# Kernel tuning notes

Hardware: AMD Instinct MI355X
Metric: run time of the kernel (lower is better)

The kernel has to match this reference:

```python
import jax, jax.numpy as jnp
import numpy as np

N, K, DIM, A, M = 20000, 16, 256, 128, 2500
EPS = 1e-5
SCALE = float(np.sqrt(A))


def _ln(x, g, b):
    mu = x.mean(-1, keepdims=True)
    var = x.var(-1, keepdims=True)
    return (x - mu) / jnp.sqrt(var + EPS) * g + b


def _pe(x, w1, b1, w2, b2):
    # PositionEncoder: Linear -> ReLU -> Linear
    return jax.nn.relu(x @ w1 + b1) @ w2 + b2


def setup_inputs() -> dict:
    key = jax.random.key(0)
    ks = jax.random.split(key, 24)
    w = lambda k, s, fan: jax.random.normal(k, s, jnp.float32) / np.sqrt(fan)
    inp = {
        'events': jax.random.normal(ks[0], (N, 4), jnp.float32),
        'features': jax.random.normal(ks[1], (N, DIM), jnp.float32),
        'local_idx': jax.random.randint(ks[2], (N, K), 0, N, jnp.int32),
        'down_idx': jax.random.randint(ks[3], (M,), 0, N, jnp.int32),
        'pair_idx': jax.random.randint(ks[4], (M, K), 0, N, jnp.int32),
        'inv_pair_idx': jax.random.randint(ks[5], (N, K), 0, M, jnp.int32),
        'local_qkv_w': w(ks[6], (DIM, 3 * A), DIM), 'local_qkv_b': jnp.zeros((3 * A,), jnp.float32),
        'local_pe_w1': w(ks[7], (4, A), 4), 'local_pe_b1': jnp.zeros((A,), jnp.float32),
        'local_pe_w2': w(ks[8], (A, A), A), 'local_pe_b2': jnp.zeros((A,), jnp.float32),
        'local_fc_g': jnp.ones((A,), jnp.float32), 'local_fc_b': jnp.zeros((A,), jnp.float32),
        'global_qkv_w': w(ks[9], (DIM, 3 * A), DIM), 'global_qkv_b': jnp.zeros((3 * A,), jnp.float32),
        'global_pe_w1': w(ks[10], (4, A), 4), 'global_pe_b1': jnp.zeros((A,), jnp.float32),
        'global_pe_w2': w(ks[11], (A, A), A), 'global_pe_b2': jnp.zeros((A,), jnp.float32),
        'global_fc_g': jnp.ones((A,), jnp.float32), 'global_fc_b': jnp.zeros((A,), jnp.float32),
        'proj_w1': w(ks[12], (2 * A, DIM), 2 * A), 'proj_b1': jnp.zeros((DIM,), jnp.float32),
        'proj_w2': w(ks[13], (DIM, DIM), DIM), 'proj_b2': jnp.zeros((DIM,), jnp.float32),
    }
    return inp


def _local_attn(events, features, local_idx, qkv_w, qkv_b,
                pe_w1, pe_b1, pe_w2, pe_b2, fc_g, fc_b):
    # pos enc on event-coordinate differences to the 16 knn neighbors
    pe = _pe(events[:, None, :] - events[local_idx], pe_w1, pe_b1, pe_w2, pe_b2)  # [N,K,A]
    qkv = features @ qkv_w + qkv_b
    q, k, v = jnp.split(qkv, 3, axis=-1)               # [N,A] each
    kg, vg = k[local_idx], v[local_idx]                # [N,K,A]
    attn = _ln(q[:, None, :] - kg + pe, fc_g, fc_b) / SCALE
    attn = jax.nn.softmax(attn, axis=1)                # softmax over neighbors
    return jnp.sum(attn * (vg + pe), axis=1)           # [N,A]


def _global_attn(events, features, down_idx, pair_idx, inv_pair_idx,
                 qkv_w, qkv_b, pe_w1, pe_b1, pe_w2, pe_b2, fc_g, fc_b):
    down_events = events[down_idx]                     # [M,4]
    pe = _pe(events[:, None, :] - down_events[inv_pair_idx], pe_w1, pe_b1, pe_w2, pe_b2)  # [N,K,A]
    qkv = features @ qkv_w + qkv_b
    q, k, v = jnp.split(qkv, 3, axis=-1)
    kmax = jnp.max(k[pair_idx], axis=1)                # [M,A] pooled over k support pts
    vmax = jnp.max(v[pair_idx], axis=1)
    kg, vg = kmax[inv_pair_idx], vmax[inv_pair_idx]    # [N,K,A]
    attn = _ln(q[:, None, :] - kg + pe, fc_g, fc_b) / SCALE
    attn = jax.nn.softmax(attn, axis=1)
    return jnp.sum(attn * (vg + pe), axis=1)


def reference(events, features, local_idx, down_idx, pair_idx, inv_pair_idx,
              local_qkv_w, local_qkv_b, local_pe_w1, local_pe_b1, local_pe_w2, local_pe_b2,
              local_fc_g, local_fc_b,
              global_qkv_w, global_qkv_b, global_pe_w1, global_pe_b1, global_pe_w2, global_pe_b2,
              global_fc_g, global_fc_b,
              proj_w1, proj_b1, proj_w2, proj_b2):
    la = _local_attn(events, features, local_idx, local_qkv_w, local_qkv_b,
                     local_pe_w1, local_pe_b1, local_pe_w2, local_pe_b2,
                     local_fc_g, local_fc_b)
    ga = _global_attn(events, features, down_idx, pair_idx, inv_pair_idx,
                      global_qkv_w, global_qkv_b, global_pe_w1, global_pe_b1,
                      global_pe_w2, global_pe_b2, global_fc_g, global_fc_b)
    attn = jnp.concatenate([la, ga], axis=-1)          # [N,2A]
    # proj MLP: Linear -> ReLU -> Linear
    return jax.nn.relu(attn @ proj_w1 + proj_b1) @ proj_w2 + proj_b2
```

## Files before the change

### kernel.cpp

```cpp
#include <hip/hip_runtime.h>

#define N_PTS 20000
#define KNN   16
#define DIMF  256
#define AD    128
#define MD    2500
#define EPSV  1e-5f
#define INV_SCALE 0.08838834764831845f
#define NEG_BIG -3.402823466e38f

typedef __attribute__((ext_vector_type(8))) short short8v;
typedef __attribute__((ext_vector_type(4))) float f32x4;

__device__ __forceinline__ float b2f(unsigned short u) {
  union { unsigned int i; float f; } v; v.i = ((unsigned int)u) << 16; return v.f;
}
__device__ __forceinline__ unsigned short f2b(float f) {
  union { float f; unsigned int i; } v; v.f = f;
  unsigned int x = v.i;
  return (unsigned short)((x + 0x7fffu + ((x >> 16) & 1u)) >> 16);
}

__global__ void EventAttention_54382875902362_kernel(float* out) {
  if (threadIdx.x == 0 && blockIdx.x == 0) out[0] = 8192.0f;
}

__global__ void prep_w2(const float* __restrict__ w2l, const float* __restrict__ w2g,
                        unsigned short* __restrict__ w2B)
{
  int id  = blockIdx.x * 256 + threadIdx.x;
  int br  = id >> 14;
  int rem = id & 16383;
  int e  = rem & 7;
  int l  = (rem >> 3) & 63;
  int ks = (rem >> 9) & 3;
  int tt = rem >> 11;
  int n = tt * 16 + (l & 15);
  int i = ks * 32 + (l >> 4) * 8 + e;
  const float* src = br ? w2g : w2l;
  w2B[id] = f2b(src[i * AD + n]);
}

__global__ void prep_frag(const float* __restrict__ src, unsigned short* __restrict__ dst,
                          int ncols, int frag_elems)
{
  int id = blockIdx.x * 256 + threadIdx.x;
  if (id >= frag_elems) return;
  int e  = id & 7;
  int l  = (id >> 3) & 63;
  int ks = (id >> 9) & 7;
  int tt = id >> 12;
  int n = tt * 16 + (l & 15);
  int k = ks * 32 + (l >> 4) * 8 + e;
  float v = src[k * ncols + n];
  unsigned short hi = f2b(v);
  unsigned short lo = f2b(v - b2f(hi));
  dst[id] = hi;
  dst[frag_elems + id] = lo;
}

__global__ void qkv_mfma(const float* __restrict__ feat,
                         const unsigned short* __restrict__ wfl, const float* __restrict__ bl,
                         const unsigned short* __restrict__ wfg, const float* __restrict__ bg,
                         float* __restrict__ qkv_l, float* __restrict__ qkv_g)
{
  __shared__ __align__(16) unsigned short aHi[16 * 256];
  __shared__ __align__(16) unsigned short aLo[16 * 256];
  const int tid  = threadIdx.x;
  const int lane = tid & 63;
  const int wv   = tid >> 6;
  const int br   = blockIdx.x & 1;
  const int row0 = (blockIdx.x >> 1) * 16;

  {
    int r = tid >> 4, seg = tid & 15;
    const float4* src = (const float4*)(feat + (size_t)(row0 + r) * 256 + seg * 16);
    #pragma unroll
    for (int q4 = 0; q4 < 4; ++q4) {
      float4 f = src[q4];
      int byte = (r * 512 + (seg * 16 + q4 * 4) * 2) ^ ((r & 7) << 4);
      ushort4 h, l2;
      h.x = f2b(f.x); l2.x = f2b(f.x - b2f(h.x));
      h.y = f2b(f.y); l2.y = f2b(f.y - b2f(h.y));
      h.z = f2b(f.z); l2.z = f2b(f.z - b2f(h.z));
      h.w = f2b(f.w); l2.w = f2b(f.w - b2f(h.w));
      *(ushort4*)((char*)aHi + byte) = h;
      *(ushort4*)((char*)aLo + byte) = l2;
    }
  }
  __syncthreads();

  short8v ah[8], al[8];
  #pragma unroll
  for (int ks = 0; ks < 8; ++ks) {
    int base = ((lane & 15) * 512 + ks * 64 + (lane >> 4) * 16) ^ ((lane & 7) << 4);
    ah[ks] = *(const short8v*)((const char*)aHi + base);
    al[ks] = *(const short8v*)((const char*)aLo + base);
  }
  const unsigned short* wf = br ? wfg : wfl;
  const float* bias        = br ? bg : bl;
  float* outp              = br ? qkv_g : qkv_l;
  const short8v* wH = (const short8v*)wf;
  const short8v* wL = wH + 12288;
  f32x4 acc[6];
  #pragma unroll
  for (int t = 0; t < 6; ++t) acc[t] = (f32x4){0.f, 0.f, 0.f, 0.f};
  #pragma unroll
  for (int t = 0; t < 6; ++t) {
    int tt = wv * 6 + t;
    #pragma unroll
    for (int ks = 0; ks < 8; ++ks) {
      short8v bh = wH[(tt * 8 + ks) * 64 + lane];
      short8v bo = wL[(tt * 8 + ks) * 64 + lane];
      acc[t] = __builtin_amdgcn_mfma_f32_16x16x32_bf16(ah[ks], bh, acc[t], 0, 0, 0);
      acc[t] = __builtin_amdgcn_mfma_f32_16x16x32_bf16(al[ks], bh, acc[t], 0, 0, 0);
      acc[t] = __builtin_amdgcn_mfma_f32_16x16x32_bf16(ah[ks], bo, acc[t], 0, 0, 0);
    }
  }
  #pragma unroll
  for (int t = 0; t < 6; ++t) {
    int colb = (wv * 6 + t) * 16 + (lane & 15);
    float bv = bias[colb];
    #pragma unroll
    for (int r = 0; r < 4; ++r) {
      int row = (lane >> 4) * 4 + r;
      outp[(size_t)(row0 + row) * 384 + colb] = acc[t][r] + bv;
    }
  }
}

__global__ void kvmax_kernel(const float* __restrict__ qkv_g,
                             const int* __restrict__ pair_idx,
                             float* __restrict__ kmax, float* __restrict__ vmax)
{
  const int m = blockIdx.x, a = threadIdx.x;
  float km = NEG_BIG, vm = NEG_BIG;
  for (int j = 0; j < KNN; ++j) {
    int p = pair_idx[m * KNN + j];
    km = fmaxf(km, qkv_g[(size_t)p * 384 + 128 + a]);
    vm = fmaxf(vm, qkv_g[(size_t)p * 384 + 256 + a]);
  }
  kmax[m * AD + a] = km;
  vmax[m * AD + a] = vm;
}

__global__ void attn_kernel(const float* __restrict__ events,
                            const int* __restrict__ idx,
                            const int* __restrict__ remap, int use_remap,
                            const float* __restrict__ q_tab, int qstride,
                            const float* __restrict__ k_tab, int kstride,
                            const float* __restrict__ v_tab, int vstride,
                            const float* __restrict__ w1, const float* __restrict__ b1,
                            const unsigned short* __restrict__ w2B, const float* __restrict__ b2,
                            const float* __restrict__ g,  const float* __restrict__ bb,
                            float* __restrict__ out, int out_off)
{
  __shared__ __align__(16) unsigned short hB[KNN * AD];
  __shared__ float scratch[KNN * 132];
  __shared__ float dS[KNN][4];
  __shared__ int   idxS[KNN];
  __shared__ float red[2][KNN][2];

  const int n    = blockIdx.x;
  const int a    = threadIdx.x;
  const int lane = a & 63;
  const int wv   = a >> 6;

  if (a < KNN * 4) {
    int j = a >> 2, c = a & 3;
    int id = idx[n * KNN + j];
    if (c == 0) idxS[j] = id;
    int erow = use_remap ? remap[id] : id;
    dS[j][c] = events[(size_t)n * 4 + c] - events[(size_t)erow * 4 + c];
  }
  const float w1r0 = w1[0 * AD + a];
  const float w1r1 = w1[1 * AD + a];
  const float w1r2 = w1[2 * AD + a];
  const float w1r3 = w1[3 * AD + a];
  const float b1r = b1[a];
  const float b2r = b2[a];
  __syncthreads();

  #pragma unroll
  for (int j = 0; j < KNN; ++j) {
    float h = b1r;
    h = fmaf(dS[j][0], w1r0, h);
    h = fmaf(dS[j][1], w1r1, h);
    h = fmaf(dS[j][2], w1r2, h);
    h = fmaf(dS[j][3], w1r3, h);
    h = fmaxf(h, 0.f);
    int byte = (j * 256 + a * 2) ^ ((j & 7) << 4);
    *(unsigned short*)((char*)hB + byte) = f2b(h);
  }
  __syncthreads();

  short8v af[4];
  #pragma unroll
  for (int ks = 0; ks < 4; ++ks) {
    int base = ((lane & 15) * 256 + ks * 64 + (lane >> 4) * 16) ^ ((lane & 7) << 4);
    af[ks] = *(const short8v*)((const char*)hB + base);
  }
  f32x4 acc[4];
  #pragma unroll
  for (int t = 0; t < 4; ++t) acc[t] = (f32x4){0.f, 0.f, 0.f, 0.f};
  const short8v* wf = (const short8v*)w2B;
  #pragma unroll
  for (int t = 0; t < 4; ++t) {
    #pragma unroll
    for (int ks = 0; ks < 4; ++ks) {
      short8v bf = wf[(((wv * 4 + t) * 4 + ks) * 64) + lane];
      acc[t] = __builtin_amdgcn_mfma_f32_16x16x32_bf16(af[ks], bf, acc[t], 0, 0, 0);
    }
  }
  #pragma unroll
  for (int t = 0; t < 4; ++t) {
    #pragma unroll
    for (int r = 0; r < 4; ++r) {
      int row = (lane >> 4) * 4 + r;
      int col = wv * 64 + t * 16 + (lane & 15);
      scratch[row * 132 + col] = acc[t][r];
    }
  }
  __syncthreads();

  float pe[KNN];
  #pragma unroll
  for (int j = 0; j < KNN; ++j) pe[j] = scratch[j * 132 + a] + b2r;

  const float qv = q_tab[(size_t)n * qstride + a];
  float x[KNN];
  #pragma unroll
  for (int j = 0; j < KNN; ++j) {
    float kg = k_tab[(size_t)idxS[j] * kstride + a];
    x[j] = qv - kg + pe[j];
  }
  __syncthreads();

  #pragma unroll
  for (int j = 0; j < KNN; ++j) scratch[j * 129 + a] = x[j];
  __syncthreads();

  {
    int jj = a & 15, pp = a >> 4;
    float s1 = 0.f, s2 = 0.f;
    #pragma unroll
    for (int c = 0; c < 16; ++c) {
      float v = scratch[jj * 129 + pp * 16 + c];
      s1 += v;
      s2 += v * v;
    }
    s1 += __shfl_xor(s1, 16, 64); s2 += __shfl_xor(s2, 16, 64);
    s1 += __shfl_xor(s1, 32, 64); s2 += __shfl_xor(s2, 32, 64);
    if (lane < 16) { red[wv][jj][0] = s1; red[wv][jj][1] = s2; }
  }
  __syncthreads();

  const float gr = g[a], br = bb[a];
  float mx = NEG_BIG;
  #pragma unroll
  for (int j = 0; j < KNN; ++j) {
    float S1 = red[0][j][0] + red[1][j][0];
    float S2 = red[0][j][1] + red[1][j][1];
    float mu  = S1 * (1.f / AD);
    float var = S2 * (1.f / AD) - mu * mu;
    float rs  = rsqrtf(var + EPSV);
    float s = ((x[j] - mu) * rs * gr + br) * INV_SCALE;
    x[j] = s;
    mx = fmaxf(mx, s);
  }
  float sum = 0.f;
  #pragma unroll
  for (int j = 0; j < KNN; ++j) {
    float p = __expf(x[j] - mx);
    x[j] = p;
    sum += p;
  }
  const float inv = 1.f / sum;
  float o = 0.f;
  #pragma unroll
  for (int j = 0; j < KNN; ++j) {
    float vg = v_tab[(size_t)idxS[j] * vstride + a];
    o += x[j] * (vg + pe[j]);
  }
  out[(size_t)n * 256 + out_off + a] = o * inv;
}

__global__ void proj_mfma(const float* __restrict__ attn_cat,
                          const unsigned short* __restrict__ w1f, const float* __restrict__ b1,
                          const unsigned short* __restrict__ w2f, const float* __restrict__ b2,
                          float* __restrict__ outp)
{
  __shared__ __align__(16) unsigned short aHi[16 * 256];
  __shared__ __align__(16) unsigned short aLo[16 * 256];
  const int tid  = threadIdx.x;
  const int lane = tid & 63;
  const int wv   = tid >> 6;
  const int row0 = blockIdx.x * 16;

  {
    int r = tid >> 4, seg = tid & 15;
    const float4* src = (const float4*)(attn_cat + (size_t)(row0 + r) * 256 + seg * 16);
    #pragma unroll
    for (int q4 = 0; q4 < 4; ++q4) {
      float4 f = src[q4];
      int byte = (r * 512 + (seg * 16 + q4 * 4) * 2) ^ ((r & 7) << 4);
      ushort4 h, l2;
      h.x = f2b(f.x); l2.x = f2b(f.x - b2f(h.x));
      h.y = f2b(f.y); l2.y = f2b(f.y - b2f(h.y));
      h.z = f2b(f.z); l2.z = f2b(f.z - b2f(h.z));
      h.w = f2b(f.w); l2.w = f2b(f.w - b2f(h.w));
      *(ushort4*)((char*)aHi + byte) = h;
      *(ushort4*)((char*)aLo + byte) = l2;
    }
  }
  __syncthreads();

  short8v ah[8], al[8];
  #pragma unroll
  for (int ks = 0; ks < 8; ++ks) {
    int base = ((lane & 15) * 512 + ks * 64 + (lane >> 4) * 16) ^ ((lane & 7) << 4);
    ah[ks] = *(const short8v*)((const char*)aHi + base);
    al[ks] = *(const short8v*)((const char*)aLo + base);
  }
  __syncthreads();

  const short8v* w1H = (const short8v*)w1f;
  const short8v* w1L = w1H + 8192;
  f32x4 acc[4];
  #pragma unroll
  for (int t = 0; t < 4; ++t) acc[t] = (f32x4){0.f, 0.f, 0.f, 0.f};
  #pragma unroll
  for (int t = 0; t < 4; ++t) {
    int tt = wv * 4 + t;
    #pragma unroll
    for (int ks = 0; ks < 8; ++ks) {
      short8v bh = w1H[(tt * 8 + ks) * 64 + lane];
      short8v bo = w1L[(tt * 8 + ks) * 64 + lane];
      acc[t] = __builtin_amdgcn_mfma_f32_16x16x32_bf16(ah[ks], bh, acc[t], 0, 0, 0);
      acc[t] = __builtin_amdgcn_mfma_f32_16x16x32_bf16(al[ks], bh, acc[t], 0, 0, 0);
      acc[t] = __builtin_amdgcn_mfma_f32_16x16x32_bf16(ah[ks], bo, acc[t], 0, 0, 0);
    }
  }
  #pragma unroll
  for (int t = 0; t < 4; ++t) {
    int col = (wv * 4 + t) * 16 + (lane & 15);
    float bv = b1[col];
    #pragma unroll
    for (int r = 0; r < 4; ++r) {
      int row = (lane >> 4) * 4 + r;
      float h = fmaxf(acc[t][r] + bv, 0.f);
      unsigned short hi = f2b(h);
      unsigned short lo = f2b(h - b2f(hi));
      int byte = (row * 512 + col * 2) ^ ((row & 7) << 4);
      *(unsigned short*)((char*)aHi + byte) = hi;
      *(unsigned short*)((char*)aLo + byte) = lo;
    }
  }
  __syncthreads();

  #pragma unroll
  for (int ks = 0; ks < 8; ++ks) {
    int base = ((lane & 15) * 512 + ks * 64 + (lane >> 4) * 16) ^ ((lane & 7) << 4);
    ah[ks] = *(const short8v*)((const char*)aHi + base);
    al[ks] = *(const short8v*)((const char*)aLo + base);
  }
  const short8v* w2H = (const short8v*)w2f;
  const short8v* w2L = w2H + 8192;
  #pragma unroll
  for (int t = 0; t < 4; ++t) acc[t] = (f32x4){0.f, 0.f, 0.f, 0.f};
  #pragma unroll
  for (int t = 0; t < 4; ++t) {
    int tt = wv * 4 + t;
    #pragma unroll
    for (int ks = 0; ks < 8; ++ks) {
      short8v bh = w2H[(tt * 8 + ks) * 64 + lane];
      short8v bo = w2L[(tt * 8 + ks) * 64 + lane];
      acc[t] = __builtin_amdgcn_mfma_f32_16x16x32_bf16(ah[ks], bh, acc[t], 0, 0, 0);
      acc[t] = __builtin_amdgcn_mfma_f32_16x16x32_bf16(al[ks], bh, acc[t], 0, 0, 0);
      acc[t] = __builtin_amdgcn_mfma_f32_16x16x32_bf16(ah[ks], bo, acc[t], 0, 0, 0);
    }
  }
  #pragma unroll
  for (int t = 0; t < 4; ++t) {
    int col = (wv * 4 + t) * 16 + (lane & 15);
    float bv = b2[col];
    #pragma unroll
    for (int r = 0; r < 4; ++r) {
      int row = (lane >> 4) * 4 + r;
      outp[(size_t)(row0 + row) * 256 + col] = acc[t][r] + bv;
    }
  }
}

extern "C" void kernel_launch(void* const* d_in, const int* in_sizes, int n_in,
                              void* d_out, int out_size, void* d_ws, size_t ws_size,
                              hipStream_t stream)
{
  const float* events   = (const float*)d_in[0];
  const float* features = (const float*)d_in[1];
  const int* local_idx    = (const int*)d_in[2];
  const int* down_idx     = (const int*)d_in[3];
  const int* pair_idx     = (const int*)d_in[4];
  const int* inv_pair_idx = (const int*)d_in[5];
  const float* l_qkv_w = (const float*)d_in[6];
  const float* l_qkv_b = (const float*)d_in[7];
  const float* l_pe_w1 = (const float*)d_in[8];
  const float* l_pe_b1 = (const float*)d_in[9];
  const float* l_pe_w2 = (const float*)d_in[10];
  const float* l_pe_b2 = (const float*)d_in[11];
  const float* l_fc_g  = (const float*)d_in[12];
  const float* l_fc_b  = (const float*)d_in[13];
  const float* g_qkv_w = (const float*)d_in[14];
  const float* g_qkv_b = (const float*)d_in[15];
  const float* g_pe_w1 = (const float*)d_in[16];
  const float* g_pe_b1 = (const float*)d_in[17];
  const float* g_pe_w2 = (const float*)d_in[18];
  const float* g_pe_b2 = (const float*)d_in[19];
  const float* g_fc_g  = (const float*)d_in[20];
  const float* g_fc_b  = (const float*)d_in[21];
  const float* p_w1 = (const float*)d_in[22];
  const float* p_b1 = (const float*)d_in[23];
  const float* p_w2 = (const float*)d_in[24];
  const float* p_b2 = (const float*)d_in[25];
  (void)in_sizes; (void)n_in; (void)out_size; (void)ws_size;

  char* ws = (char*)d_ws;
  size_t off = 0;
  float* qkv_l    = (float*)(ws + off); off += (size_t)N_PTS * 384 * 4;
  float* qkv_g    = (float*)(ws + off); off += (size_t)N_PTS * 384 * 4;
  float* kmax     = (float*)(ws + off); off += (size_t)MD * AD * 4;
  float* vmax     = (float*)(ws + off); off += (size_t)MD * AD * 4;
  float* attn_cat = (float*)(ws + off); off += (size_t)N_PTS * 256 * 4;
  unsigned short* w2B   = (unsigned short*)(ws + off); off += 32768 * 2;
  unsigned short* wfL   = (unsigned short*)(ws + off); off += 196608 * 2;
  unsigned short* wfG   = (unsigned short*)(ws + off); off += 196608 * 2;
  unsigned short* wp1   = (unsigned short*)(ws + off); off += 131072 * 2;
  unsigned short* wp2   = (unsigned short*)(ws + off); off += 131072 * 2;

  EventAttention_54382875902362_kernel<<<1, 64, 0, stream>>>((float*)d_out);
  prep_w2<<<128, 256, 0, stream>>>(l_pe_w2, g_pe_w2, w2B);
  prep_frag<<<384, 256, 0, stream>>>(l_qkv_w, wfL, 384, 98304);
  prep_frag<<<384, 256, 0, stream>>>(g_qkv_w, wfG, 384, 98304);
  prep_frag<<<256, 256, 0, stream>>>(p_w1, wp1, 256, 65536);
  prep_frag<<<256, 256, 0, stream>>>(p_w2, wp2, 256, 65536);

  qkv_mfma<<<2500, 256, 0, stream>>>(
      features, wfL, l_qkv_b, wfG, g_qkv_b, qkv_l, qkv_g);
  kvmax_kernel<<<MD, 128, 0, stream>>>(qkv_g, pair_idx, kmax, vmax);
  attn_kernel<<<N_PTS, 128, 0, stream>>>(
      events, local_idx, down_idx, 0,
      qkv_l + 0, 384, qkv_l + 128, 384, qkv_l + 256, 384,
      l_pe_w1, l_pe_b1, w2B, l_pe_b2, l_fc_g, l_fc_b,
      attn_cat, 0);
  attn_kernel<<<N_PTS, 128, 0, stream>>>(
      events, inv_pair_idx, down_idx, 1,
      qkv_g + 0, 384, kmax, 128, vmax, 128,
      g_pe_w1, g_pe_b1, w2B + 16384, g_pe_b2, g_fc_g, g_fc_b,
      attn_cat, 128);
  proj_mfma<<<N_PTS / 16, 256, 0, stream>>>(
      attn_cat, wp1, p_b1, wp2, p_b2, (float*)d_out);
}
```

Before: 235.8 us.

## Rewrite attention kernel as single-wave block computing in MFMA accumulator layout

Shrinks the attention kernel from 128 to 64 threads per point so one wavefront does all 8 MFMA output tiles. LayerNorm, softmax and the weighted V sum now run directly on the accumulator fragments, with wave shuffles replacing the shared-memory scratch transposes and block reductions. This removes several __syncthreads and LDS round trips per point. The cost is more registers per thread, and the K/V gathers now use a 16-lane-strided access pattern.

```diff
diff --git a/kernel.cpp b/kernel.cpp
--- a/kernel.cpp
+++ b/kernel.cpp
@@ -156,133 +156,149 @@
                             float* __restrict__ out, int out_off)
 {
   __shared__ __align__(16) unsigned short hB[KNN * AD];
-  __shared__ float scratch[KNN * 132];
   __shared__ float dS[KNN][4];
   __shared__ int   idxS[KNN];
-  __shared__ float red[2][KNN][2];
-
-  const int n    = blockIdx.x;
-  const int a    = threadIdx.x;
-  const int lane = a & 63;
-  const int wv   = a >> 6;
-
-  if (a < KNN * 4) {
-    int j = a >> 2, c = a & 3;
+
+  const int n  = blockIdx.x;
+  const int l  = threadIdx.x;
+  const int lg = l >> 4;
+  const int li = l & 15;
+
+  {
+    int j = l >> 2, c = l & 3;
     int id = idx[n * KNN + j];
     if (c == 0) idxS[j] = id;
     int erow = use_remap ? remap[id] : id;
     dS[j][c] = events[(size_t)n * 4 + c] - events[(size_t)erow * 4 + c];
   }
-  const float w1r0 = w1[0 * AD + a];
-  const float w1r1 = w1[1 * AD + a];
-  const float w1r2 = w1[2 * AD + a];
-  const float w1r3 = w1[3 * AD + a];
-  const float b1r = b1[a];
-  const float b2r = b2[a];
+
+  float w1r[4][2];
+  #pragma unroll
+  for (int c = 0; c < 4; ++c) {
+    w1r[c][0] = w1[c * AD + 2 * l];
+    w1r[c][1] = w1[c * AD + 2 * l + 1];
+  }
+  const float b1r0 = b1[2 * l], b1r1 = b1[2 * l + 1];
+  float b2v[8], gv[8], bv[8], qv[8];
+  #pragma unroll
+  for (int tt = 0; tt < 8; ++tt) {
+    int c = tt * 16 + li;
+    b2v[tt] = b2[c];
+    gv[tt]  = g[c];
+    bv[tt]  = bb[c];
+    qv[tt]  = q_tab[(size_t)n * qstride + c];
+  }
   __syncthreads();
 
   #pragma unroll
   for (int j = 0; j < KNN; ++j) {
-    float h = b1r;
-    h = fmaf(dS[j][0], w1r0, h);
-    h = fmaf(dS[j][1], w1r1, h);
-    h = fmaf(dS[j][2], w1r2, h);
-    h = fmaf(dS[j][3], w1r3, h);
-    h = fmaxf(h, 0.f);
-    int byte = (j * 256 + a * 2) ^ ((j & 7) << 4);
-    *(unsigned short*)((char*)hB + byte) = f2b(h);
+    const float4 d = *(const float4*)dS[j];
+    float h0 = b1r0, h1 = b1r1;
+    h0 = fmaf(d.x, w1r[0][0], h0); h1 = fmaf(d.x, w1r[0][1], h1);
+    h0 = fmaf(d.y, w1r[1][0], h0); h1 = fmaf(d.y, w1r[1][1], h1);
+    h0 = fmaf(d.z, w1r[2][0], h0); h1 = fmaf(d.z, w1r[2][1], h1);
+    h0 = fmaf(d.w, w1r[3][0], h0); h1 = fmaf(d.w, w1r[3][1], h1);
+    h0 = fmaxf(h0, 0.f); h1 = fmaxf(h1, 0.f);
+    unsigned int packed = (unsigned int)f2b(h0) | ((unsigned int)f2b(h1) << 16);
+    int byte = (j * 256 + l * 4) ^ ((j & 7) << 4);
+    *(unsigned int*)((char*)hB + byte) = packed;
   }
   __syncthreads();
 
   short8v af[4];
   #pragma unroll
   for (int ks = 0; ks < 4; ++ks) {
-    int base = ((lane & 15) * 256 + ks * 64 + (lane >> 4) * 16) ^ ((lane & 7) << 4);
+    int base = (li * 256 + ks * 64 + lg * 16) ^ ((li & 7) << 4);
     af[ks] = *(const short8v*)((const char*)hB + base);
   }
-  f32x4 acc[4];
-  #pragma unroll
-  for (int t = 0; t < 4; ++t) acc[t] = (f32x4){0.f, 0.f, 0.f, 0.f};
+  f32x4 acc[8];
+  #pragma unroll
+  for (int tt = 0; tt < 8; ++tt) acc[tt] = (f32x4){0.f, 0.f, 0.f, 0.f};
   const short8v* wf = (const short8v*)w2B;
   #pragma unroll
-  for (int t = 0; t < 4; ++t) {
+  for (int tt = 0; tt < 8; ++tt) {
     #pragma unroll
     for (int ks = 0; ks < 4; ++ks) {
-      short8v bf = wf[(((wv * 4 + t) * 4 + ks) * 64) + lane];
-      acc[t] = __builtin_amdgcn_mfma_f32_16x16x32_bf16(af[ks], bf, acc[t], 0, 0, 0);
-    }
-  }
-  #pragma unroll
-  for (int t = 0; t < 4; ++t) {
+      short8v bf = wf[(tt * 4 + ks) * 64 + l];
+      acc[tt] = __builtin_amdgcn_mfma_f32_16x16x32_bf16(af[ks], bf, acc[tt], 0, 0, 0);
+    }
+  }
+  #pragma unroll
+  for (int tt = 0; tt < 8; ++tt) {
+    #pragma unroll
+    for (int r = 0; r < 4; ++r) acc[tt][r] += b2v[tt];
+  }
+
+  const float* kbase[4];
+  #pragma unroll
+  for (int r = 0; r < 4; ++r)
+    kbase[r] = k_tab + (size_t)idxS[4 * lg + r] * kstride + li;
+  float x[8][4];
+  #pragma unroll
+  for (int tt = 0; tt < 8; ++tt) {
+    #pragma unroll
+    for (int r = 0; r < 4; ++r)
+      x[tt][r] = qv[tt] - kbase[r][tt * 16] + acc[tt][r];
+  }
+
+  float mu_[4], rs_[4];
+  #pragma unroll
+  for (int r = 0; r < 4; ++r) {
+    float s1 = 0.f, s2 = 0.f;
+    #pragma unroll
+    for (int tt = 0; tt < 8; ++tt) {
+      float v = x[tt][r];
+      s1 += v;
+      s2 = fmaf(v, v, s2);
+    }
+    s1 += __shfl_xor(s1, 1, 64);  s2 += __shfl_xor(s2, 1, 64);
+    s1 += __shfl_xor(s1, 2, 64);  s2 += __shfl_xor(s2, 2, 64);
+    s1 += __shfl_xor(s1, 4, 64);  s2 += __shfl_xor(s2, 4, 64);
+    s1 += __shfl_xor(s1, 8, 64);  s2 += __shfl_xor(s2, 8, 64);
+    float mu  = s1 * (1.f / AD);
+    float var = s2 * (1.f / AD) - mu * mu;
+    mu_[r] = mu;
+    rs_[r] = rsqrtf(var + EPSV);
+  }
+  #pragma unroll
+  for (int tt = 0; tt < 8; ++tt) {
+    #pragma unroll
+    for (int r = 0; r < 4; ++r)
+      x[tt][r] = (fmaf((x[tt][r] - mu_[r]) * rs_[r], gv[tt], bv[tt])) * INV_SCALE;
+  }
+
+  float sm[8];
+  #pragma unroll
+  for (int tt = 0; tt < 8; ++tt) {
+    float m0 = fmaxf(fmaxf(x[tt][0], x[tt][1]), fmaxf(x[tt][2], x[tt][3]));
+    m0 = fmaxf(m0, __shfl_xor(m0, 16, 64));
+    m0 = fmaxf(m0, __shfl_xor(m0, 32, 64));
+    float s = 0.f;
     #pragma unroll
     for (int r = 0; r < 4; ++r) {
-      int row = (lane >> 4) * 4 + r;
-      int col = wv * 64 + t * 16 + (lane & 15);
-      scratch[row * 132 + col] = acc[t][r];
-    }
-  }
-  __syncthreads();
-
-  float pe[KNN];
-  #pragma unroll
-  for (int j = 0; j < KNN; ++j) pe[j] = scratch[j * 132 + a] + b2r;
-
-  const float qv = q_tab[(size_t)n * qstride + a];
-  float x[KNN];
-  #pragma unroll
-  for (int j = 0; j < KNN; ++j) {
-    float kg = k_tab[(size_t)idxS[j] * kstride + a];
-    x[j] = qv - kg + pe[j];
-  }
-  __syncthreads();
-
-  #pragma unroll
-  for (int j = 0; j < KNN; ++j) scratch[j * 129 + a] = x[j];
-  __syncthreads();
-
-  {
-    int jj = a & 15, pp = a >> 4;
-    float s1 = 0.f, s2 = 0.f;
-    #pragma unroll
-    for (int c = 0; c < 16; ++c) {
-      float v = scratch[jj * 129 + pp * 16 + c];
-      s1 += v;
-      s2 += v * v;
-    }
-    s1 += __shfl_xor(s1, 16, 64); s2 += __shfl_xor(s2, 16, 64);
-    s1 += __shfl_xor(s1, 32, 64); s2 += __shfl_xor(s2, 32, 64);
-    if (lane < 16) { red[wv][jj][0] = s1; red[wv][jj][1] = s2; }
-  }
-  __syncthreads();
-
-  const float gr = g[a], br = bb[a];
-  float mx = NEG_BIG;
-  #pragma unroll
-  for (int j = 0; j < KNN; ++j) {
-    float S1 = red[0][j][0] + red[1][j][0];
-    float S2 = red[0][j][1] + red[1][j][1];
-    float mu  = S1 * (1.f / AD);
-    float var = S2 * (1.f / AD) - mu * mu;
-    float rs  = rsqrtf(var + EPSV);
-    float s = ((x[j] - mu) * rs * gr + br) * INV_SCALE;
-    x[j] = s;
-    mx = fmaxf(mx, s);
-  }
-  float sum = 0.f;
-  #pragma unroll
-  for (int j = 0; j < KNN; ++j) {
-    float p = __expf(x[j] - mx);
-    x[j] = p;
-    sum += p;
-  }
-  const float inv = 1.f / sum;
-  float o = 0.f;
-  #pragma unroll
-  for (int j = 0; j < KNN; ++j) {
-    float vg = v_tab[(size_t)idxS[j] * vstride + a];
-    o += x[j] * (vg + pe[j]);
-  }
-  out[(size_t)n * 256 + out_off + a] = o * inv;
+      x[tt][r] = __expf(x[tt][r] - m0);
+      s += x[tt][r];
+    }
+    s += __shfl_xor(s, 16, 64);
+    s += __shfl_xor(s, 32, 64);
+    sm[tt] = s;
+  }
+
+  const float* vbase[4];
+  #pragma unroll
+  for (int r = 0; r < 4; ++r)
+    vbase[r] = v_tab + (size_t)idxS[4 * lg + r] * vstride + li;
+  #pragma unroll
+  for (int tt = 0; tt < 8; ++tt) {
+    float o = 0.f;
+    #pragma unroll
+    for (int r = 0; r < 4; ++r)
+      o = fmaf(x[tt][r], vbase[r][tt * 16] + acc[tt][r], o);
+    o += __shfl_xor(o, 16, 64);
+    o += __shfl_xor(o, 32, 64);
+    if (lg == 0)
+      out[(size_t)n * 256 + out_off + tt * 16 + li] = o / sm[tt];
+  }
 }
 
 __global__ void proj_mfma(const float* __restrict__ attn_cat,
@@ -344,11 +360,11 @@
   #pragma unroll
   for (int t = 0; t < 4; ++t) {
     int col = (wv * 4 + t) * 16 + (lane & 15);
-    float bv = b1[col];
+    float bvv = b1[col];
     #pragma unroll
     for (int r = 0; r < 4; ++r) {
       int row = (lane >> 4) * 4 + r;
-      float h = fmaxf(acc[t][r] + bv, 0.f);
+      float h = fmaxf(acc[t][r] + bvv, 0.f);
       unsigned short hi = f2b(h);
       unsigned short lo = f2b(h - b2f(hi));
       int byte = (row * 512 + col * 2) ^ ((row & 7) << 4);
@@ -383,11 +399,11 @@
   #pragma unroll
   for (int t = 0; t < 4; ++t) {
     int col = (wv * 4 + t) * 16 + (lane & 15);
-    float bv = b2[col];
+    float bvv = b2[col];
     #pragma unroll
     for (int r = 0; r < 4; ++r) {
       int row = (lane >> 4) * 4 + r;
-      outp[(size_t)(row0 + row) * 256 + col] = acc[t][r] + bv;
+      outp[(size_t)(row0 + row) * 256 + col] = acc[t][r] + bvv;
     }
   }
 }
@@ -447,12 +463,12 @@
   qkv_mfma<<<2500, 256, 0, stream>>>(
       features, wfL, l_qkv_b, wfG, g_qkv_b, qkv_l, qkv_g);
   kvmax_kernel<<<MD, 128, 0, stream>>>(qkv_g, pair_idx, kmax, vmax);
-  attn_kernel<<<N_PTS, 128, 0, stream>>>(
+  attn_kernel<<<N_PTS, 64, 0, stream>>>(
       events, local_idx, down_idx, 0,
       qkv_l + 0, 384, qkv_l + 128, 384, qkv_l + 256, 384,
       l_pe_w1, l_pe_b1, w2B, l_pe_b2, l_fc_g, l_fc_b,
       attn_cat, 0);
-  attn_kernel<<<N_PTS, 128, 0, stream>>>(
+  attn_kernel<<<N_PTS, 64, 0, stream>>>(
       events, inv_pair_idx, down_idx, 1,
       qkv_g + 0, 384, kmax, 128, vmax, 128,
       g_pe_w1, g_pe_b1, w2B + 16384, g_pe_b2, g_fc_g, g_fc_b,
```

New measurement: 248.3 us. +5.3%, slower.

## Merge local and global attention launches and prefetch gathered K/V early

Applied to the files above, without the earlier changes.

The two attention launches become one grid of 2*N blocks, with even blocks taking the local branch and odd blocks the global branch, selected by pointer choice. Each thread now loads its neighbor indices and gathers the K and V rows into registers at kernel start, so those global loads overlap the positional-encoding MLP and MFMA work instead of waiting on it. The LayerNorm scale is folded into gamma and beta and a few multiply-adds are turned into fma. The cost is higher register pressure from the 32 extra per-thread values and mixed branch behaviour within one grid.

```diff
diff --git a/kernel.cpp b/kernel.cpp
--- a/kernel.cpp
+++ b/kernel.cpp
@@ -144,33 +144,60 @@
   vmax[m * AD + a] = vm;
 }
 
-__global__ void attn_kernel(const float* __restrict__ events,
-                            const int* __restrict__ idx,
-                            const int* __restrict__ remap, int use_remap,
-                            const float* __restrict__ q_tab, int qstride,
-                            const float* __restrict__ k_tab, int kstride,
-                            const float* __restrict__ v_tab, int vstride,
-                            const float* __restrict__ w1, const float* __restrict__ b1,
-                            const unsigned short* __restrict__ w2B, const float* __restrict__ b2,
-                            const float* __restrict__ g,  const float* __restrict__ bb,
-                            float* __restrict__ out, int out_off)
+__global__ void attn_fused(const float* __restrict__ events,
+                           const int* __restrict__ local_idx,
+                           const int* __restrict__ inv_pair_idx,
+                           const int* __restrict__ down_idx,
+                           const float* __restrict__ qkv_l,
+                           const float* __restrict__ qkv_g,
+                           const float* __restrict__ kmax,
+                           const float* __restrict__ vmax,
+                           const float* __restrict__ w1L, const float* __restrict__ b1L,
+                           const unsigned short* __restrict__ w2BL, const float* __restrict__ b2L,
+                           const float* __restrict__ gL,  const float* __restrict__ bbL,
+                           const float* __restrict__ w1G, const float* __restrict__ b1G,
+                           const unsigned short* __restrict__ w2BG, const float* __restrict__ b2G,
+                           const float* __restrict__ gG,  const float* __restrict__ bbG,
+                           float* __restrict__ out)
 {
   __shared__ __align__(16) unsigned short hB[KNN * AD];
   __shared__ float scratch[KNN * 132];
   __shared__ float dS[KNN][4];
-  __shared__ int   idxS[KNN];
   __shared__ float red[2][KNN][2];
 
-  const int n    = blockIdx.x;
+  const int bid  = blockIdx.x;
+  const int gbr  = bid & 1;
+  const int n    = bid >> 1;
   const int a    = threadIdx.x;
   const int lane = a & 63;
   const int wv   = a >> 6;
 
+  const int*   idx = gbr ? inv_pair_idx : local_idx;
+  const float* qt  = gbr ? qkv_g : qkv_l;
+  const float* kt  = gbr ? kmax : (qkv_l + 128);
+  const float* vt  = gbr ? vmax : (qkv_l + 256);
+  const int    ks_ = gbr ? 128 : 384;
+  const float* w1  = gbr ? w1G : w1L;
+  const float* b1  = gbr ? b1G : b1L;
+  const unsigned short* w2B = gbr ? w2BG : w2BL;
+  const float* b2  = gbr ? b2G : b2L;
+  const float* gg  = gbr ? gG : gL;
+  const float* bbp = gbr ? bbG : bbL;
+
+  int id[KNN];
+  #pragma unroll
+  for (int j = 0; j < KNN; ++j) id[j] = idx[n * KNN + j];
+
+  const float qv = qt[(size_t)n * 384 + a];
+  float kg[KNN], vg[KNN];
+  #pragma unroll
+  for (int j = 0; j < KNN; ++j) kg[j] = kt[(size_t)id[j] * ks_ + a];
+  #pragma unroll
+  for (int j = 0; j < KNN; ++j) vg[j] = vt[(size_t)id[j] * ks_ + a];
+
   if (a < KNN * 4) {
     int j = a >> 2, c = a & 3;
-    int id = idx[n * KNN + j];
-    if (c == 0) idxS[j] = id;
-    int erow = use_remap ? remap[id] : id;
+    int erow = gbr ? down_idx[id[j]] : id[j];
     dS[j][c] = events[(size_t)n * 4 + c] - events[(size_t)erow * 4 + c];
   }
   const float w1r0 = w1[0 * AD + a];
@@ -179,15 +206,18 @@
   const float w1r3 = w1[3 * AD + a];
   const float b1r = b1[a];
   const float b2r = b2[a];
+  const float gr  = gg[a] * INV_SCALE;
+  const float brv = bbp[a] * INV_SCALE;
   __syncthreads();
 
   #pragma unroll
   for (int j = 0; j < KNN; ++j) {
+    const float4 d = *(const float4*)dS[j];
     float h = b1r;
-    h = fmaf(dS[j][0], w1r0, h);
-    h = fmaf(dS[j][1], w1r1, h);
-    h = fmaf(dS[j][2], w1r2, h);
-    h = fmaf(dS[j][3], w1r3, h);
+    h = fmaf(d.x, w1r0, h);
+    h = fmaf(d.y, w1r1, h);
+    h = fmaf(d.z, w1r2, h);
+    h = fmaf(d.w, w1r3, h);
     h = fmaxf(h, 0.f);
     int byte = (j * 256 + a * 2) ^ ((j & 7) << 4);
     *(unsigned short*)((char*)hB + byte) = f2b(h);
@@ -196,9 +226,9 @@
 
   short8v af[4];
   #pragma unroll
-  for (int ks = 0; ks < 4; ++ks) {
-    int base = ((lane & 15) * 256 + ks * 64 + (lane >> 4) * 16) ^ ((lane & 7) << 4);
-    af[ks] = *(const short8v*)((const char*)hB + base);
+  for (int ksl = 0; ksl < 4; ++ksl) {
+    int base = ((lane & 15) * 256 + ksl * 64 + (lane >> 4) * 16) ^ ((lane & 7) << 4);
+    af[ksl] = *(const short8v*)((const char*)hB + base);
   }
   f32x4 acc[4];
   #pragma unroll
@@ -207,9 +237,9 @@
   #pragma unroll
   for (int t = 0; t < 4; ++t) {
     #pragma unroll
-    for (int ks = 0; ks < 4; ++ks) {
-      short8v bf = wf[(((wv * 4 + t) * 4 + ks) * 64) + lane];
-      acc[t] = __builtin_amdgcn_mfma_f32_16x16x32_bf16(af[ks], bf, acc[t], 0, 0, 0);
+    for (int ksl = 0; ksl < 4; ++ksl) {
+      short8v bf = wf[(((wv * 4 + t) * 4 + ksl) * 64) + lane];
+      acc[t] = __builtin_amdgcn_mfma_f32_16x16x32_bf16(af[ksl], bf, acc[t], 0, 0, 0);
     }
   }
   #pragma unroll
@@ -223,16 +253,11 @@
   }
   __syncthreads();
 
-  float pe[KNN];
-  #pragma unroll
-  for (int j = 0; j < KNN; ++j) pe[j] = scratch[j * 132 + a] + b2r;
-
-  const float qv = q_tab[(size_t)n * qstride + a];
-  float x[KNN];
+  float pe[KNN], x[KNN];
   #pragma unroll
   for (int j = 0; j < KNN; ++j) {
-    float kg = k_tab[(size_t)idxS[j] * kstride + a];
-    x[j] = qv - kg + pe[j];
+    pe[j] = scratch[j * 132 + a] + b2r;
+    x[j]  = qv - kg[j] + pe[j];
   }
   __syncthreads();
 
@@ -247,7 +272,7 @@
     for (int c = 0; c < 16; ++c) {
       float v = scratch[jj * 129 + pp * 16 + c];
       s1 += v;
-      s2 += v * v;
+      s2 = fmaf(v, v, s2);
     }
     s1 += __shfl_xor(s1, 16, 64); s2 += __shfl_xor(s2, 16, 64);
     s1 += __shfl_xor(s1, 32, 64); s2 += __shfl_xor(s2, 32, 64);
@@ -255,7 +280,6 @@
   }
   __syncthreads();
 
-  const float gr = g[a], br = bb[a];
   float mx = NEG_BIG;
   #pragma unroll
   for (int j = 0; j < KNN; ++j) {
@@ -264,7 +288,7 @@
     float mu  = S1 * (1.f / AD);
     float var = S2 * (1.f / AD) - mu * mu;
     float rs  = rsqrtf(var + EPSV);
-    float s = ((x[j] - mu) * rs * gr + br) * INV_SCALE;
+    float s = fmaf((x[j] - mu) * rs, gr, brv);
     x[j] = s;
     mx = fmaxf(mx, s);
   }
@@ -278,11 +302,9 @@
   const float inv = 1.f / sum;
   float o = 0.f;
   #pragma unroll
-  for (int j = 0; j < KNN; ++j) {
-    float vg = v_tab[(size_t)idxS[j] * vstride + a];
-    o += x[j] * (vg + pe[j]);
-  }
-  out[(size_t)n * 256 + out_off + a] = o * inv;
+  for (int j = 0; j < KNN; ++j)
+    o = fmaf(x[j], vg[j] + pe[j], o);
+  out[(size_t)n * 256 + (gbr ? 128 : 0) + a] = o * inv;
 }
 
 __global__ void proj_mfma(const float* __restrict__ attn_cat,
@@ -344,11 +366,11 @@
   #pragma unroll
   for (int t = 0; t < 4; ++t) {
     int col = (wv * 4 + t) * 16 + (lane & 15);
-    float bv = b1[col];
+    float bvv = b1[col];
     #pragma unroll
     for (int r = 0; r < 4; ++r) {
       int row = (lane >> 4) * 4 + r;
-      float h = fmaxf(acc[t][r] + bv, 0.f);
+      float h = fmaxf(acc[t][r] + bvv, 0.f);
       unsigned short hi = f2b(h);
       unsigned short lo = f2b(h - b2f(hi));
       int byte = (row * 512 + col * 2) ^ ((row & 7) << 4);
@@ -383,11 +405,11 @@
   #pragma unroll
   for (int t = 0; t < 4; ++t) {
     int col = (wv * 4 + t) * 16 + (lane & 15);
-    float bv = b2[col];
+    float bvv = b2[col];
     #pragma unroll
     for (int r = 0; r < 4; ++r) {
       int row = (lane >> 4) * 4 + r;
-      outp[(size_t)(row0 + row) * 256 + col] = acc[t][r] + bv;
+      outp[(size_t)(row0 + row) * 256 + col] = acc[t][r] + bvv;
     }
   }
 }
@@ -447,16 +469,12 @@
   qkv_mfma<<<2500, 256, 0, stream>>>(
       features, wfL, l_qkv_b, wfG, g_qkv_b, qkv_l, qkv_g);
   kvmax_kernel<<<MD, 128, 0, stream>>>(qkv_g, pair_idx, kmax, vmax);
-  attn_kernel<<<N_PTS, 128, 0, stream>>>(
-      events, local_idx, down_idx, 0,
-      qkv_l + 0, 384, qkv_l + 128, 384, qkv_l + 256, 384,
+  attn_fused<<<2 * N_PTS, 128, 0, stream>>>(
+      events, local_idx, inv_pair_idx, down_idx,
+      qkv_l, qkv_g, kmax, vmax,
       l_pe_w1, l_pe_b1, w2B, l_pe_b2, l_fc_g, l_fc_b,
-      attn_cat, 0);
-  attn_kernel<<<N_PTS, 128, 0, stream>>>(
-      events, inv_pair_idx, down_idx, 1,
-      qkv_g + 0, 384, kmax, 128, vmax, 128,
       g_pe_w1, g_pe_b1, w2B + 16384, g_pe_b2, g_fc_g, g_fc_b,
-      attn_cat, 128);
+      attn_cat);
   proj_mfma<<<N_PTS / 16, 256, 0, stream>>>(
       attn_cat, wp1, p_b1, wp2, p_b2, (float*)d_out);
 }
```

New measurement: 244.7 us. 3.8% more time.
